# Kernel optimization log

Hardware: AMD Instinct MI355X
Metric: run time of the kernel (lower is better)

## Reference

```python
import jax, jax.numpy as jnp
import numpy as np


def group_norm(x, g, b, groups, eps=1e-5):
    # x: (B, C, H, W), PyTorch GroupNorm semantics
    B, C, H, W = x.shape
    xr = x.reshape(B, groups, -1)
    m = xr.mean(-1, keepdims=True)
    v = xr.var(-1, keepdims=True)
    xn = ((xr - m) * jax.lax.rsqrt(v + eps)).reshape(B, C, H, W)
    return xn * g[:, None, None] + b[:, None, None]


def mamba(xs, in_w, conv_w, conv_b, xproj_w, dt_w, dt_b, A_log, D, out_w):
    # Standard Mamba block: in_proj -> causal depthwise conv -> SiLU ->
    # x_proj -> softplus(dt_proj) -> selective scan -> gate -> out_proj.
    Bsz, L, d = xs.shape
    di = in_w.shape[0] // 2
    r = dt_w.shape[1]
    n = A_log.shape[1]
    K = conv_w.shape[1]
    xz = xs @ in_w.T                           # (B, L, 2*di)
    xpart, z = xz[..., :di], xz[..., di:]
    xp = jnp.pad(xpart, ((0, 0), (K - 1, 0), (0, 0)))  # causal pad
    xc = conv_b + sum(xp[:, k:k + L, :] * conv_w[:, k] for k in range(K))
    xc = jax.nn.silu(xc)
    proj = xc @ xproj_w.T                      # (B, L, r + 2n)
    dt = proj[..., :r]
    Bm = proj[..., r:r + n]
    Cm = proj[..., r + n:]
    delta = jax.nn.softplus(dt @ dt_w.T + dt_b)   # (B, L, di)
    A = -jnp.exp(A_log)                            # (di, n)
    dA = jnp.exp(jnp.einsum('bld,dn->bldn', delta, A))
    dBu = jnp.einsum('bld,bln,bld->bldn', delta, Bm, xc)

    def step(h, inp):
        dA_t, dBu_t, C_t = inp
        h = dA_t * h + dBu_t                  # (B, di, n)
        return h, jnp.einsum('bdn,bn->bd', h, C_t)

    h0 = jnp.zeros((Bsz, di, n), xs.dtype)
    _, ys = jax.lax.scan(step, h0, (jnp.moveaxis(dA, 1, 0), jnp.moveaxis(dBu, 1, 0), jnp.moveaxis(Cm, 1, 0)))
    y = jnp.moveaxis(ys, 0, 1) + D * xc
    y = y * jax.nn.silu(z)
    return y @ out_w.T


def setup_inputs() -> dict:
    def nrm(i, shape, s=0.05):
        return jax.random.normal(jax.random.fold_in(jax.random.key(0), i), shape, dtype=jnp.float32) * s

    f32 = jnp.float32
    C = 128
    di, r, n = 256, 8, 16          # spa mamba: d_model=128, expand=2
    di2, r2 = 64, 2                # spe mamba: d_model=32
    A1 = jnp.log(jnp.broadcast_to(jnp.arange(1, n + 1, dtype=f32), (di, n)))
    A2 = jnp.log(jnp.broadcast_to(jnp.arange(1, n + 1, dtype=f32), (di2, n)))
    return {
        'x': nrm(0, (2, C, 64, 64), 1.0),
        'pe_w': nrm(1, (C, C)), 'pe_b': jnp.zeros((C,), f32),
        'pe_gn_g': jnp.ones((C,), f32), 'pe_gn_b': jnp.zeros((C,), f32),
        'spa_in_w': nrm(2, (2 * di, C)),
        'spa_conv_w': nrm(3, (di, 4)), 'spa_conv_b': jnp.zeros((di,), f32),
        'spa_xproj_w': nrm(4, (r + 2 * n, di)),
        'spa_dt_w': nrm(5, (di, r)), 'spa_dt_b': jnp.full((di,), -2.0, f32),
        'spa_Alog': A1, 'spa_D': jnp.ones((di,), f32),
        'spa_out_w': nrm(6, (C, di)),
        'spa_gn_g': jnp.ones((C,), f32), 'spa_gn_b': jnp.zeros((C,), f32),
        'spe_in_w': nrm(7, (2 * di2, 32)),
        'spe_conv_w': nrm(8, (di2, 4)), 'spe_conv_b': jnp.zeros((di2,), f32),
        'spe_xproj_w': nrm(9, (r2 + 2 * n, di2)),
        'spe_dt_w': nrm(10, (di2, r2)), 'spe_dt_b': jnp.full((di2,), -2.0, f32),
        'spe_Alog': A2, 'spe_D': jnp.ones((di2,), f32),
        'spe_out_w': nrm(11, (32, di2)),
        'spe_gn_g': jnp.ones((C,), f32), 'spe_gn_b': jnp.zeros((C,), f32),
        'fuse_w': jnp.full((2,), 0.5, f32),
        'cls_w': nrm(12, (10, C)), 'cls_b': jnp.zeros((10,), f32),
        'ref_dw_w': nrm(13, (C, 1, 3, 3)),
        'ref_gn_g': jnp.ones((C,), f32), 'ref_gn_b': jnp.zeros((C,), f32),
        'ref_pw_w': nrm(14, (1, C)), 'ref_pw_b': jnp.zeros((1,), f32),
        'alpha': jnp.asarray(1e-4, f32),
    }


def reference(x, pe_w, pe_b, pe_gn_g, pe_gn_b, spa_in_w, spa_conv_w, spa_conv_b, spa_xproj_w, spa_dt_w, spa_dt_b, spa_Alog, spa_D, spa_out_w, spa_gn_g, spa_gn_b, spe_in_w, spe_conv_w, spe_conv_b, spe_xproj_w, spe_dt_w, spe_dt_b, spe_Alog, spe_D, spe_out_w, spe_gn_g, spe_gn_b, fuse_w, cls_w, cls_b, ref_dw_w, ref_gn_g, ref_gn_b, ref_pw_w, ref_pw_b, alpha):
    B, _, H, W = x.shape
    # patch embedding: 1x1 conv + GroupNorm + SiLU
    h1 = jnp.einsum('bchw,oc->bohw', x, pe_w) + pe_b[:, None, None]
    h1 = jax.nn.silu(group_norm(h1, pe_gn_g, pe_gn_b, 4))
    # SpaMamba: scan over flattened spatial tokens (B, H*W, C)
    seq = h1.transpose(0, 2, 3, 1).reshape(B, H * W, -1)
    y = mamba(seq, spa_in_w, spa_conv_w, spa_conv_b, spa_xproj_w, spa_dt_w, spa_dt_b, spa_Alog, spa_D, spa_out_w)
    y = y.reshape(B, H, W, -1).transpose(0, 3, 1, 2)
    spa = jax.nn.silu(group_norm(y, spa_gn_g, spa_gn_b, 4)) + h1
    # SpeMamba: token_num=4, group_channel_num=32, channel_num=128 (no pad)
    seq2 = h1.transpose(0, 2, 3, 1).reshape(B * H * W, 4, 32)
    y2 = mamba(seq2, spe_in_w, spe_conv_w, spe_conv_b, spe_xproj_w, spe_dt_w, spe_dt_b, spe_Alog, spe_D, spe_out_w)
    y2 = y2.reshape(B, H, W, -1).transpose(0, 3, 1, 2)
    spe = h1 + jax.nn.silu(group_norm(y2, spe_gn_g, spe_gn_b, 4))
    # attention-weighted fusion + residual (BothMamba, use_att=True)
    wts = jax.nn.softmax(fuse_w)
    feat = spa * wts[0] + spe * wts[1] + h1
    # classifier head (1x1 conv)
    logits = jnp.einsum('bchw,oc->bohw', feat, cls_w) + cls_b[:, None, None]
    # BoundaryAwareLogitRefiner
    edge = jax.lax.conv_general_dilated(feat, ref_dw_w, (1, 1), ((1, 1), (1, 1)), feature_group_count=feat.shape[1], dimension_numbers=('NCHW', 'OIHW', 'NCHW'))
    edge = jax.nn.silu(group_norm(edge, ref_gn_g, ref_gn_b, 4))
    edge = jax.nn.sigmoid(jnp.einsum('bchw,oc->bohw', edge, ref_pw_w) + ref_pw_b[:, None, None])
    local = jax.lax.reduce_window(logits, 0.0, jax.lax.add, (1, 1, 3, 3), (1, 1, 1, 1), ((0, 0), (0, 0), (1, 1), (1, 1))) / 9.0  # count_include_pad=True
    return logits + alpha * (1.0 - edge) * (local - logits)
```

## Files before the change

### kernel.cpp

```cpp
#include <hip/hip_runtime.h>
#include <math.h>

#define DEV __device__ __forceinline__

DEV float sigm(float x){ return 1.f/(1.f+__expf(-x)); }
DEV float siluf(float x){ return x * sigm(x); }
DEV float softplusf(float x){ return x > 20.f ? x : log1pf(__expf(x)); }

static constexpr float NG = 131072.0f;

static constexpr size_t WS_H1    = 0;
static constexpr size_t WS_H1PRE = 1048576;
static constexpr size_t WS_XC    = 2097152;
static constexpr size_t WS_ZSIL  = 4194304;
static constexpr size_t WS_XZ    = 6291456;
static constexpr size_t WS_DELTA = 6291456;
static constexpr size_t WS_BM    = 8388608;
static constexpr size_t WS_CM    = 8519680;
static constexpr size_t WS_LOG   = 8650752;
static constexpr size_t WS_Y     = 10485760;
static constexpr size_t WS_P     = 12582912;
static constexpr size_t WS_Q     = 13107200;
static constexpr size_t WS_HS    = 13631488;
static constexpr size_t WS_Y2    = 14155776;
static constexpr size_t WS_FEAT  = 15204352;
static constexpr size_t WS_STATS = 16252928;
static constexpr size_t WS_PEWT  = 16253056;
static constexpr size_t WS_INWT  = WS_PEWT  + 16384;
static constexpr size_t WS_OUTWT = WS_INWT  + 65536;
static constexpr size_t WS_XPWT  = WS_OUTWT + 32768;

__global__ void __launch_bounds__(256)
k_red(const float* __restrict__ part, float* __restrict__ outS, int half){
  __shared__ float red[4];
  int b = blockIdx.x >> 3, j = blockIdx.x & 7;
  float s = 0.f;
  for (int i = b*half + threadIdx.x; i < (b+1)*half; i += 256)
    s += part[(size_t)i*8 + j];
  s += __shfl_xor(s,1); s += __shfl_xor(s,2); s += __shfl_xor(s,4);
  s += __shfl_xor(s,8); s += __shfl_xor(s,16); s += __shfl_xor(s,32);
  if ((threadIdx.x & 63) == 0) red[threadIdx.x>>6] = s;
  __syncthreads();
  if (threadIdx.x == 0) outS[b*8+j] = red[0]+red[1]+red[2]+red[3];
}

__global__ void __launch_bounds__(256)
k_transpose(const float* __restrict__ pe_w, const float* __restrict__ in_w,
            const float* __restrict__ out_w, const float* __restrict__ xp_w,
            float* __restrict__ peT, float* __restrict__ inT,
            float* __restrict__ outT, float* __restrict__ xpT){
  int i0 = blockIdx.x*256 + threadIdx.x;
  int nt = gridDim.x*256;
  for (int k = i0; k < 128*128; k += nt){ int r = k >> 7, c = k & 127; peT[c*128 + r] = pe_w[k]; }
  for (int k = i0; k < 512*128; k += nt){ int r = k >> 7, c = k & 127; inT[c*512 + r] = in_w[k]; }
  for (int k = i0; k < 128*256; k += nt){ int r = k >> 8, c = k & 255; outT[c*128 + r] = out_w[k]; }
  for (int k = i0; k < 40*256;  k += nt){ int r = k >> 8, c = k & 255; xpT[c*40 + r] = xp_w[k]; }
}

__global__ void __launch_bounds__(256)
k_pe(const float* __restrict__ x, const float* __restrict__ peT,
     const float* __restrict__ pe_b, float* __restrict__ h1pre,
     float* __restrict__ part){
  __shared__ float xs[128][33];
  __shared__ float red1[4][64], red2[4][64];
  int tid = threadIdx.x;
  int m0 = blockIdx.x * 32;
  int b = m0 >> 12, pl = m0 & 4095;
  for (int i = tid; i < 32*128; i += 256){
    int t = i >> 7, c = i & 127;
    xs[c][t] = x[(size_t)(b*128 + c)*4096 + pl + t];
  }
  __syncthreads();
  int o = tid & 127, half = tid >> 7;
  float acc[16];
  #pragma unroll
  for (int t = 0; t < 16; t++) acc[t] = 0.f;
  for (int c = 0; c < 128; c++){
    float wv = peT[c*128 + o];
    const float* xr = &xs[c][half*16];
    #pragma unroll
    for (int t = 0; t < 16; t++) acc[t] += wv * xr[t];
  }
  float bo = pe_b[o];
  float s1 = 0.f, s2 = 0.f;
  for (int t = 0; t < 16; t++){
    float vv = acc[t] + bo;
    s1 += vv; s2 += vv*vv;
    h1pre[(size_t)(m0 + half*16 + t)*128 + o] = vv;
  }
  int g = o >> 5, idx = (o & 31) | (half << 5);
  red1[g][idx] = s1; red2[g][idx] = s2;
  __syncthreads();
  int rg = tid >> 6, ridx = tid & 63;
  for (int s = 32; s >= 1; s >>= 1){
    if (ridx < s){ red1[rg][ridx] += red1[rg][ridx+s]; red2[rg][ridx] += red2[rg][ridx+s]; }
    __syncthreads();
  }
  if (ridx == 0){
    part[(size_t)blockIdx.x*8 + rg*2+0] = red1[rg][0];
    part[(size_t)blockIdx.x*8 + rg*2+1] = red2[rg][0];
  }
}

__global__ void __launch_bounds__(256)
k_gnsilu(const float* __restrict__ pre, const float* __restrict__ stats,
         const float* __restrict__ gw, const float* __restrict__ gb,
         float* __restrict__ outb){
  int idx = blockIdx.x*256 + threadIdx.x;
  int c = idx & 127; int pix = idx >> 7; int b = pix >> 12; int g = c >> 5;
  float s1 = stats[(b*4+g)*2], s2 = stats[(b*4+g)*2+1];
  float m = s1 * (1.f/NG);
  float v = s2 * (1.f/NG) - m*m;
  float xn = (pre[idx] - m) * rsqrtf(v + 1e-5f);
  float val = xn * gw[c] + gb[c];
  outb[idx] = siluf(val);
}

__global__ void __launch_bounds__(256)
k_xz(const float* __restrict__ h1, const float* __restrict__ inT,
     float* __restrict__ xz){
  __shared__ float xs[128][33];
  int tid = threadIdx.x;
  int m0 = blockIdx.x * 32;
  for (int i = tid; i < 32*128; i += 256){
    int t = i >> 7, c = i & 127;
    xs[c][t] = h1[(size_t)(m0 + t)*128 + c];
  }
  __syncthreads();
  float acc0[32], acc1[32];
  #pragma unroll
  for (int t = 0; t < 32; t++){ acc0[t]=0.f; acc1[t]=0.f; }
  int o = tid;
  for (int c = 0; c < 128; c++){
    float w0 = inT[c*512 + o];
    float w1 = inT[c*512 + o + 256];
    #pragma unroll
    for (int t = 0; t < 32; t++){
      float a = xs[c][t];
      acc0[t] += w0*a; acc1[t] += w1*a;
    }
  }
  for (int t = 0; t < 32; t++){
    xz[(size_t)(m0+t)*512 + o]       = acc0[t];
    xz[(size_t)(m0+t)*512 + o + 256] = acc1[t];
  }
}

__global__ void __launch_bounds__(256)
k_conv(const float* __restrict__ xz, const float* __restrict__ cw,
       const float* __restrict__ cb, float* __restrict__ xc,
       float* __restrict__ zsil){
  int idx = blockIdx.x*256 + threadIdx.x;
  int d = idx & 255;
  int l = (idx >> 8) & 4095;
  int b = idx >> 20;
  float v = cb[d];
  #pragma unroll
  for (int k = 0; k < 4; k++){
    int ls = l - 3 + k;
    if (ls >= 0) v += xz[(size_t)(b*4096 + ls)*512 + d] * cw[d*4 + k];
  }
  xc[idx] = siluf(v);
  float z = xz[(size_t)(b*4096 + l)*512 + 256 + d];
  zsil[idx] = siluf(z);
}

__global__ void __launch_bounds__(256)
k_proj(const float* __restrict__ xc, const float* __restrict__ xpT,
       const float* __restrict__ dtw, const float* __restrict__ dtb,
       float* __restrict__ delta, float* __restrict__ Bm, float* __restrict__ Cm){
  __shared__ float xt[32][260];
  __shared__ float pr[32][40];
  int tid = threadIdx.x;
  int m0 = blockIdx.x * 32;
  for (int i = tid; i < 32*256; i += 256){
    int t = i >> 8, d = i & 255;
    xt[t][d] = xc[(size_t)(m0+t)*256 + d];
  }
  __syncthreads();
  {
    int t = tid >> 3, j0 = tid & 7;
    float a0=0.f,a1=0.f,a2=0.f,a3=0.f,a4=0.f;
    for (int d = 0; d < 256; d++){
      float xv = xt[t][d];
      const float* wp = &xpT[d*40 + j0];
      a0 += xv*wp[0]; a1 += xv*wp[8]; a2 += xv*wp[16]; a3 += xv*wp[24]; a4 += xv*wp[32];
    }
    pr[t][j0] = a0; pr[t][j0+8] = a1; pr[t][j0+16] = a2; pr[t][j0+24] = a3; pr[t][j0+32] = a4;
  }
  __syncthreads();
  {
    int d = tid;
    float w[8];
    #pragma unroll
    for (int r = 0; r < 8; r++) w[r] = dtw[d*8+r];
    float bd = dtb[d];
    for (int t = 0; t < 32; t++){
      float val = bd;
      #pragma unroll
      for (int r = 0; r < 8; r++) val += pr[t][r]*w[r];
      delta[(size_t)(m0+t)*256 + d] = softplusf(val);
    }
  }
  for (int i = tid; i < 512; i += 256){
    int t = i >> 4, n = i & 15;
    Bm[(size_t)(m0+t)*16 + n] = pr[t][8+n];
    Cm[(size_t)(m0+t)*16 + n] = pr[t][24+n];
  }
}

__global__ void __launch_bounds__(256)
k_scan1(const float* __restrict__ delta, const float* __restrict__ xc,
        const float* __restrict__ Bm, const float* __restrict__ Alog,
        float* __restrict__ P, float* __restrict__ Q){
  __shared__ float sd[64][16], sx[64][16], sb[64][16];
  int blk = blockIdx.x;
  int b = blk >> 10;
  int chunk = (blk >> 4) & 63;
  int dblk = blk & 15;
  int tid = threadIdx.x;
  size_t rowbase = (size_t)(b*4096 + chunk*64);
  for (int i = tid; i < 64*16; i += 256){
    int ii = i >> 4, dd = i & 15;
    sd[ii][dd] = delta[(rowbase + ii)*256 + dblk*16 + dd];
    sx[ii][dd] = xc  [(rowbase + ii)*256 + dblk*16 + dd];
    sb[ii][dd] = Bm  [(rowbase + ii)*16 + dd];
  }
  int dl = tid >> 4, n = tid & 15;
  int d = dblk*16 + dl;
  float An = -__expf(Alog[d*16 + n]);
  __syncthreads();
  float Pv = 1.f, Qv = 0.f;
  for (int i = 0; i < 64; i++){
    float dv = sd[i][dl];
    float a = __expf(dv * An);
    Qv = a*Qv + dv * sb[i][n] * sx[i][dl];
    Pv *= a;
  }
  size_t o = (size_t)(b*64+chunk)*4096 + dblk*256 + tid;
  P[o] = Pv; Q[o] = Qv;
}

__global__ void __launch_bounds__(256)
k_scan2(const float* __restrict__ P, const float* __restrict__ Q,
        float* __restrict__ hs){
  int gid = blockIdx.x*256 + threadIdx.x;
  int b = gid >> 12, dn = gid & 4095;
  float h = 0.f;
  for (int ch = 0; ch < 64; ch++){
    size_t idx = (size_t)(b*64 + ch)*4096 + dn;
    hs[idx] = h;
    h = P[idx]*h + Q[idx];
  }
}

__global__ void __launch_bounds__(256)
k_scan3(const float* __restrict__ delta, const float* __restrict__ xc,
        const float* __restrict__ Bm, const float* __restrict__ Cm,
        const float* __restrict__ zsil, const float* __restrict__ Alog,
        const float* __restrict__ Dv, const float* __restrict__ hs,
        float* __restrict__ y){
  __shared__ float sd[64][16], sx[64][16], sb[64][16], sc[64][16], sz[64][16], yt[64][16];
  int blk = blockIdx.x;
  int b = blk >> 10;
  int chunk = (blk >> 4) & 63;
  int dblk = blk & 15;
  int tid = threadIdx.x;
  size_t rowbase = (size_t)(b*4096 + chunk*64);
  for (int i = tid; i < 64*16; i += 256){
    int ii = i >> 4, dd = i & 15;
    sd[ii][dd] = delta[(rowbase + ii)*256 + dblk*16 + dd];
    sx[ii][dd] = xc  [(rowbase + ii)*256 + dblk*16 + dd];
    sz[ii][dd] = zsil[(rowbase + ii)*256 + dblk*16 + dd];
    sb[ii][dd] = Bm  [(rowbase + ii)*16 + dd];
    sc[ii][dd] = Cm  [(rowbase + ii)*16 + dd];
  }
  int dl = tid >> 4, n = tid & 15;
  int d = dblk*16 + dl;
  float An = -__expf(Alog[d*16 + n]);
  float h = hs[(size_t)(b*64+chunk)*4096 + dblk*256 + tid];
  float Dd = Dv[d];
  __syncthreads();
  for (int i = 0; i < 64; i++){
    float dv = sd[i][dl], xv = sx[i][dl];
    float a = __expf(dv * An);
    h = a*h + dv * sb[i][n] * xv;
    float ctr = h * sc[i][n];
    ctr += __shfl_xor(ctr, 1);
    ctr += __shfl_xor(ctr, 2);
    ctr += __shfl_xor(ctr, 4);
    ctr += __shfl_xor(ctr, 8);
    if (n == 0) yt[i][dl] = (ctr + Dd*xv) * sz[i][dl];
  }
  __syncthreads();
  for (int i = tid; i < 1024; i += 256){
    int ii = i >> 4, dd = i & 15;
    y[(rowbase + ii)*256 + dblk*16 + dd] = yt[ii][dd];
  }
}

__global__ void __launch_bounds__(256)
k_outproj(const float* __restrict__ y, const float* __restrict__ outT,
          float* __restrict__ yproj, float* __restrict__ part){
  __shared__ float ytile[256][33];
  __shared__ float red1[4][64], red2[4][64];
  int tid = threadIdx.x;
  int m0 = blockIdx.x * 32;
  for (int i = tid; i < 32*256; i += 256){
    int t = i >> 8, d = i & 255;
    ytile[d][t] = y[(size_t)(m0+t)*256 + d];
  }
  __syncthreads();
  int o = tid & 127, half = tid >> 7;
  float acc[16];
  #pragma unroll
  for (int t = 0; t < 16; t++) acc[t] = 0.f;
  for (int d = 0; d < 256; d++){
    float wv = outT[d*128 + o];
    const float* yr = &ytile[d][half*16];
    #pragma unroll
    for (int t = 0; t < 16; t++) acc[t] += wv * yr[t];
  }
  float s1 = 0.f, s2 = 0.f;
  for (int t = 0; t < 16; t++){
    float vv = acc[t];
    s1 += vv; s2 += vv*vv;
    yproj[(size_t)(m0 + half*16 + t)*128 + o] = vv;
  }
  int g = o >> 5, idx = (o & 31) | (half << 5);
  red1[g][idx] = s1; red2[g][idx] = s2;
  __syncthreads();
  int rg = tid >> 6, ridx = tid & 63;
  for (int s = 32; s >= 1; s >>= 1){
    if (ridx < s){ red1[rg][ridx] += red1[rg][ridx+s]; red2[rg][ridx] += red2[rg][ridx+s]; }
    __syncthreads();
  }
  if (ridx == 0){
    part[(size_t)blockIdx.x*8 + rg*2+0] = red1[rg][0];
    part[(size_t)blockIdx.x*8 + rg*2+1] = red2[rg][0];
  }
}

__global__ void __launch_bounds__(256)
k_spe_a(const float* __restrict__ h1, const float* __restrict__ in_w,
        const float* __restrict__ conv_w, const float* __restrict__ conv_b,
        float* __restrict__ xc2, float* __restrict__ xc2T,
        float* __restrict__ zsil2){
  __shared__ float s_in[4][128];
  int tid = threadIdx.x;
  int w = tid >> 6, lane = tid & 63;
  float wx[32], wz[32];
  {
    const float4* rx = (const float4*)(in_w + (size_t)lane*32);
    const float4* rz = (const float4*)(in_w + (size_t)(64+lane)*32);
    #pragma unroll
    for (int k = 0; k < 8; k++){
      float4 a = rx[k]; wx[k*4]=a.x; wx[k*4+1]=a.y; wx[k*4+2]=a.z; wx[k*4+3]=a.w;
      float4 b = rz[k]; wz[k*4]=b.x; wz[k*4+1]=b.y; wz[k*4+2]=b.z; wz[k*4+3]=b.w;
    }
  }
  float4 cwv = ((const float4*)conv_w)[lane];
  float cbv = conv_b[lane];
  for (int i = 0; i < 4; i++){
    int pix = blockIdx.x*16 + w*4 + i;
    float2 hv = ((const float2*)(h1 + (size_t)pix*128))[lane];
    s_in[w][2*lane] = hv.x; s_in[w][2*lane+1] = hv.y;
    float xpr[4], zs[4];
    #pragma unroll
    for (int l = 0; l < 4; l++){
      const float4* sv = (const float4*)&s_in[w][l*32];
      float ax = 0.f, az = 0.f;
      #pragma unroll
      for (int c4 = 0; c4 < 8; c4++){
        float4 v = sv[c4];
        ax += v.x*wx[c4*4] + v.y*wx[c4*4+1] + v.z*wx[c4*4+2] + v.w*wx[c4*4+3];
        az += v.x*wz[c4*4] + v.y*wz[c4*4+1] + v.z*wz[c4*4+2] + v.w*wz[c4*4+3];
      }
      xpr[l] = ax; zs[l] = siluf(az);
    }
    #pragma unroll
    for (int l = 0; l < 4; l++){
      float v = cbv;
      if (l >= 3) v += xpr[l-3]*cwv.x;
      if (l >= 2) v += xpr[l-2]*cwv.y;
      if (l >= 1) v += xpr[l-1]*cwv.z;
      v += xpr[l]*cwv.w;
      float sx = siluf(v);
      int tok = pix*4 + l;
      xc2 [(size_t)tok*64 + lane] = sx;
      xc2T[(size_t)lane*32768 + tok] = sx;
      zsil2[(size_t)tok*64 + lane] = zs[l];
    }
  }
}

__global__ void __launch_bounds__(256)
k_spe_b(const float* __restrict__ xc2T, const float* __restrict__ xpw,
        float* __restrict__ proj){
  int tok = blockIdx.x*256 + threadIdx.x;
  float xcv[64];
  #pragma unroll 64
  for (int dd = 0; dd < 64; dd++) xcv[dd] = xc2T[(size_t)dd*32768 + tok];
  float* pr = proj + (size_t)tok*36;
  #pragma unroll 2
  for (int j = 0; j < 34; j++){
    const float4* wr = (const float4*)(xpw + j*64);
    float a = 0.f;
    #pragma unroll
    for (int k = 0; k < 16; k++){
      float4 wv = wr[k];
      a += xcv[k*4]*wv.x + xcv[k*4+1]*wv.y + xcv[k*4+2]*wv.z + xcv[k*4+3]*wv.w;
    }
    pr[j] = a;
  }
}

__global__ void __launch_bounds__(256)
k_spe_c(const float* __restrict__ xc2, const float* __restrict__ zsil2,
        const float* __restrict__ proj, const float* __restrict__ dt_w,
        const float* __restrict__ dt_b, const float* __restrict__ Alog,
        const float* __restrict__ Dvec, float* __restrict__ yg){
  int tid = threadIdx.x;
  int w = tid >> 6, lane = tid & 63;
  float2 dtwv = ((const float2*)dt_w)[lane];
  float dbv = dt_b[lane], Dd = Dvec[lane];
  float An[16];
  {
    const float4* ar = (const float4*)(Alog + (size_t)lane*16);
    #pragma unroll
    for (int k = 0; k < 4; k++){
      float4 a = ar[k];
      An[k*4]   = -__expf(a.x); An[k*4+1] = -__expf(a.y);
      An[k*4+2] = -__expf(a.z); An[k*4+3] = -__expf(a.w);
    }
  }
  for (int i = 0; i < 4; i++){
    int pix = blockIdx.x*16 + w*4 + i;
    float h[16];
    #pragma unroll
    for (int n = 0; n < 16; n++) h[n] = 0.f;
    #pragma unroll
    for (int l = 0; l < 4; l++){
      int tok = pix*4 + l;
      float pj[36];
      {
        const float4* pr = (const float4*)(proj + (size_t)tok*36);
        #pragma unroll
        for (int k = 0; k < 9; k++){
          float4 v = pr[k];
          pj[k*4]=v.x; pj[k*4+1]=v.y; pj[k*4+2]=v.z; pj[k*4+3]=v.w;
        }
      }
      float xv = xc2[(size_t)tok*64 + lane];
      float zv = zsil2[(size_t)tok*64 + lane];
      float dt = softplusf(dbv + pj[0]*dtwv.x + pj[1]*dtwv.y);
      float ys = 0.f;
      #pragma unroll
      for (int n = 0; n < 16; n++){
        float a = __expf(dt * An[n]);
        h[n] = a*h[n] + dt * pj[2+n] * xv;
        ys += h[n] * pj[18+n];
      }
      yg[(size_t)tok*64 + lane] = (ys + Dd*xv) * zv;
    }
  }
}

__global__ void __launch_bounds__(256)
k_spe_d(const float* __restrict__ yg, const float* __restrict__ out_w,
        float* __restrict__ y2, float* __restrict__ part){
  __shared__ float ldsWT[64*32];
  __shared__ float bst[8];
  int tid = threadIdx.x;
  for (int i = tid; i < 2048; i += 256){
    int c2 = i >> 6, dd = i & 63;
    ldsWT[dd*32 + c2] = out_w[i];
  }
  if (tid < 8) bst[tid] = 0.f;
  __syncthreads();
  int w = tid >> 6, lane = tid & 63;
  int c2 = lane & 31, slot = lane >> 5;
  int tokbase = blockIdx.x*64 + w*16 + slot;
  float acc[8];
  #pragma unroll
  for (int i = 0; i < 8; i++) acc[i] = 0.f;
  for (int dd4 = 0; dd4 < 16; dd4++){
    float w0 = ldsWT[(dd4*4+0)*32 + c2];
    float w1 = ldsWT[(dd4*4+1)*32 + c2];
    float w2 = ldsWT[(dd4*4+2)*32 + c2];
    float w3 = ldsWT[(dd4*4+3)*32 + c2];
    #pragma unroll
    for (int i = 0; i < 8; i++){
      int tok = tokbase + 2*i;
      float4 yv = ((const float4*)(yg + (size_t)tok*64))[dd4];
      acc[i] += yv.x*w0 + yv.y*w1 + yv.z*w2 + yv.w*w3;
    }
  }
  #pragma unroll
  for (int i = 0; i < 8; i++){
    int tok = tokbase + 2*i;
    int pix = tok >> 2, l = tok & 3;
    y2[(size_t)pix*128 + l*32 + c2] = acc[i];
    float s1 = acc[i], s2 = acc[i]*acc[i];
    s1 += __shfl_xor(s1,1);  s2 += __shfl_xor(s2,1);
    s1 += __shfl_xor(s1,2);  s2 += __shfl_xor(s2,2);
    s1 += __shfl_xor(s1,4);  s2 += __shfl_xor(s2,4);
    s1 += __shfl_xor(s1,8);  s2 += __shfl_xor(s2,8);
    s1 += __shfl_xor(s1,16); s2 += __shfl_xor(s2,16);
    if (c2 == 0){
      atomicAdd(&bst[l*2+0], s1);
      atomicAdd(&bst[l*2+1], s2);
    }
  }
  __syncthreads();
  if (tid < 8) part[(size_t)blockIdx.x*8 + tid] = bst[tid];
}

__global__ void __launch_bounds__(256)
k_fuse(const float* __restrict__ h1, const float* __restrict__ yproj,
       const float* __restrict__ y2, const float* __restrict__ stats,
       const float* __restrict__ spa_g, const float* __restrict__ spa_b,
       const float* __restrict__ spe_g, const float* __restrict__ spe_b,
       const float* __restrict__ fuse_w, const float* __restrict__ cls_w,
       const float* __restrict__ cls_b, float* __restrict__ feat,
       float* __restrict__ logits){
  __shared__ float ft[2][128];
  int tid = threadIdx.x;
  int pixl = tid >> 7, c = tid & 127;
  int pix = blockIdx.x*2 + pixl;
  int b = pix >> 12, g = c >> 5;
  float m1 = stats[16 + (b*4+g)*2]   * (1.f/NG);
  float v1 = stats[16 + (b*4+g)*2+1] * (1.f/NG) - m1*m1;
  float m2 = stats[32 + (b*4+g)*2]   * (1.f/NG);
  float v2 = stats[32 + (b*4+g)*2+1] * (1.f/NG) - m2*m2;
  float h = h1[(size_t)pix*128 + c];
  float sa = siluf((yproj[(size_t)pix*128+c] - m1)*rsqrtf(v1+1e-5f)*spa_g[c] + spa_b[c]) + h;
  float sp = h + siluf((y2[(size_t)pix*128+c] - m2)*rsqrtf(v2+1e-5f)*spe_g[c] + spe_b[c]);
  float e0 = __expf(fuse_w[0]), e1 = __expf(fuse_w[1]);
  float w0 = e0/(e0+e1), w1 = e1/(e0+e1);
  float f = sa*w0 + sp*w1 + h;
  feat[(size_t)pix*128+c] = f;
  ft[pixl][c] = f;
  __syncthreads();
  if (tid < 20){
    int pl = (tid >= 10) ? 1 : 0;
    int o = tid - pl*10;
    float acc = cls_b[o];
    for (int cc = 0; cc < 128; cc++) acc += ft[pl][cc]*cls_w[o*128+cc];
    logits[(size_t)(blockIdx.x*2 + pl)*16 + o] = acc;
  }
}

__global__ void __launch_bounds__(256)
k_dw(const float* __restrict__ feat, const float* __restrict__ dww,
     float* __restrict__ epre, float* __restrict__ part){
  __shared__ float red1[4][64], red2[4][64];
  int tid = threadIdx.x;
  int pixl = tid >> 7, c = tid & 127;
  int pix = blockIdx.x*2 + pixl;
  int b = pix >> 12, p = pix & 4095, yy = p >> 6, xx = p & 63;
  float acc = 0.f;
  for (int dy = -1; dy <= 1; dy++){
    int ny = yy + dy; if (ny < 0 || ny > 63) continue;
    for (int dx = -1; dx <= 1; dx++){
      int nx = xx + dx; if (nx < 0 || nx > 63) continue;
      acc += feat[(size_t)((b<<12)|(ny<<6)|nx)*128 + c] * dww[c*9 + (dy+1)*3 + (dx+1)];
    }
  }
  epre[(size_t)pix*128 + c] = acc;
  int g = c >> 5;
  int idx = (c & 31) | (pixl << 5);
  red1[g][idx] = acc; red2[g][idx] = acc*acc;
  __syncthreads();
  int rg = tid >> 6, ridx = tid & 63;
  for (int s = 32; s >= 1; s >>= 1){
    if (ridx < s){ red1[rg][ridx] += red1[rg][ridx+s]; red2[rg][ridx] += red2[rg][ridx+s]; }
    __syncthreads();
  }
  if (ridx == 0){
    part[(size_t)blockIdx.x*8 + rg*2+0] = red1[rg][0];
    part[(size_t)blockIdx.x*8 + rg*2+1] = red2[rg][0];
  }
}

__global__ void __launch_bounds__(256)
k_final(const float* __restrict__ epre, const float* __restrict__ logits,
        const float* __restrict__ stats, const float* __restrict__ rg_g,
        const float* __restrict__ rg_b, const float* __restrict__ pw_w,
        const float* __restrict__ pw_b, const float* __restrict__ alpha,
        float* __restrict__ outp){
  __shared__ float part[4];
  __shared__ float edge_s[2];
  int tid = threadIdx.x;
  int pixl = tid >> 7, c = tid & 127;
  int pix = blockIdx.x*2 + pixl;
  int b = pix >> 12, p = pix & 4095, yy = p >> 6, xx = p & 63;
  int g = c >> 5;
  float m = stats[48 + (b*4+g)*2]   * (1.f/NG);
  float v = stats[48 + (b*4+g)*2+1] * (1.f/NG) - m*m;
  float e = epre[(size_t)pix*128+c];
  float en = siluf((e-m)*rsqrtf(v+1e-5f)*rg_g[c] + rg_b[c]);
  float pv = en * pw_w[c];
  pv += __shfl_xor(pv,1);  pv += __shfl_xor(pv,2);  pv += __shfl_xor(pv,4);
  pv += __shfl_xor(pv,8);  pv += __shfl_xor(pv,16); pv += __shfl_xor(pv,32);
  if ((tid & 63) == 0) part[tid>>6] = pv;
  __syncthreads();
  if (tid < 2) edge_s[tid] = sigm(part[tid*2] + part[tid*2+1] + pw_b[0]);
  __syncthreads();
  if (c < 10){
    float ed = edge_s[pixl];
    int o = c;
    float lg = logits[(size_t)pix*16 + o];
    float loc = 0.f;
    for (int dy = -1; dy <= 1; dy++){
      int ny = yy+dy; if (ny < 0 || ny > 63) continue;
      for (int dx = -1; dx <= 1; dx++){
        int nx = xx+dx; if (nx < 0 || nx > 63) continue;
        loc += logits[(size_t)((b<<12)|(ny<<6)|nx)*16 + o];
      }
    }
    loc *= (1.f/9.f);
    outp[(size_t)((b*10+o)<<12) + p] = lg + alpha[0]*(1.f-ed)*(loc - lg);
  }
}

extern "C" void kernel_launch(void* const* d_in, const int* in_sizes, int n_in,
                              void* d_out, int out_size, void* d_ws, size_t ws_size,
                              hipStream_t stream){
  const float* x          = (const float*)d_in[0];
  const float* pe_w       = (const float*)d_in[1];
  const float* pe_b       = (const float*)d_in[2];
  const float* pe_gn_g    = (const float*)d_in[3];
  const float* pe_gn_b    = (const float*)d_in[4];
  const float* spa_in_w   = (const float*)d_in[5];
  const float* spa_conv_w = (const float*)d_in[6];
  const float* spa_conv_b = (const float*)d_in[7];
  const float* spa_xproj_w= (const float*)d_in[8];
  const float* spa_dt_w   = (const float*)d_in[9];
  const float* spa_dt_b   = (const float*)d_in[10];
  const float* spa_Alog   = (const float*)d_in[11];
  const float* spa_D      = (const float*)d_in[12];
  const float* spa_out_w  = (const float*)d_in[13];
  const float* spa_gn_g   = (const float*)d_in[14];
  const float* spa_gn_b   = (const float*)d_in[15];
  const float* spe_in_w   = (const float*)d_in[16];
  const float* spe_conv_w = (const float*)d_in[17];
  const float* spe_conv_b = (const float*)d_in[18];
  const float* spe_xproj_w= (const float*)d_in[19];
  const float* spe_dt_w   = (const float*)d_in[20];
  const float* spe_dt_b   = (const float*)d_in[21];
  const float* spe_Alog   = (const float*)d_in[22];
  const float* spe_D      = (const float*)d_in[23];
  const float* spe_out_w  = (const float*)d_in[24];
  const float* spe_gn_g   = (const float*)d_in[25];
  const float* spe_gn_b   = (const float*)d_in[26];
  const float* fuse_w     = (const float*)d_in[27];
  const float* cls_w      = (const float*)d_in[28];
  const float* cls_b      = (const float*)d_in[29];
  const float* ref_dw_w   = (const float*)d_in[30];
  const float* ref_gn_g   = (const float*)d_in[31];
  const float* ref_gn_b   = (const float*)d_in[32];
  const float* ref_pw_w   = (const float*)d_in[33];
  const float* ref_pw_b   = (const float*)d_in[34];
  const float* alpha      = (const float*)d_in[35];
  float* ws  = (float*)d_ws;
  float* out = (float*)d_out;

  float* partPE  = ws + WS_Y;
  float* partSPA = ws + WS_HS;
  float* partSPE = ws + WS_Q;
  float* partDW  = ws + WS_P;
  float* xc2   = ws + WS_XC;
  float* xc2T  = ws + WS_ZSIL;
  float* zsil2 = ws + WS_DELTA;
  float* proj  = ws + WS_BM;
  float* yg    = ws + WS_Y;

  k_transpose<<<64,256,0,stream>>>(pe_w, spa_in_w, spa_out_w, spa_xproj_w,
      ws+WS_PEWT, ws+WS_INWT, ws+WS_OUTWT, ws+WS_XPWT);
  k_pe<<<256,256,0,stream>>>(x, ws+WS_PEWT, pe_b, ws+WS_H1PRE, partPE);
  k_red<<<16,256,0,stream>>>(partPE, ws+WS_STATS+0, 128);
  k_gnsilu<<<4096,256,0,stream>>>(ws+WS_H1PRE, ws+WS_STATS, pe_gn_g, pe_gn_b, ws+WS_H1);
  k_xz<<<256,256,0,stream>>>(ws+WS_H1, ws+WS_INWT, ws+WS_XZ);
  k_conv<<<8192,256,0,stream>>>(ws+WS_XZ, spa_conv_w, spa_conv_b, ws+WS_XC, ws+WS_ZSIL);
  k_proj<<<256,256,0,stream>>>(ws+WS_XC, ws+WS_XPWT, spa_dt_w, spa_dt_b,
      ws+WS_DELTA, ws+WS_BM, ws+WS_CM);
  k_scan1<<<2048,256,0,stream>>>(ws+WS_DELTA, ws+WS_XC, ws+WS_BM, spa_Alog, ws+WS_P, ws+WS_Q);
  k_scan2<<<32,256,0,stream>>>(ws+WS_P, ws+WS_Q, ws+WS_HS);
  k_scan3<<<2048,256,0,stream>>>(ws+WS_DELTA, ws+WS_XC, ws+WS_BM, ws+WS_CM,
      ws+WS_ZSIL, spa_Alog, spa_D, ws+WS_HS, ws+WS_Y);
  k_outproj<<<256,256,0,stream>>>(ws+WS_Y, ws+WS_OUTWT, ws+WS_H1PRE, partSPA);
  k_red<<<16,256,0,stream>>>(partSPA, ws+WS_STATS+16, 128);
  k_spe_a<<<512,256,0,stream>>>(ws+WS_H1, spe_in_w, spe_conv_w, spe_conv_b,
      xc2, xc2T, zsil2);
  k_spe_b<<<128,256,0,stream>>>(xc2T, spe_xproj_w, proj);
  k_spe_c<<<512,256,0,stream>>>(xc2, zsil2, proj, spe_dt_w, spe_dt_b,
      spe_Alog, spe_D, yg);
  k_spe_d<<<512,256,0,stream>>>(yg, spe_out_w, ws+WS_Y2, partSPE);
  k_red<<<16,256,0,stream>>>(partSPE, ws+WS_STATS+32, 256);
  k_fuse<<<4096,256,0,stream>>>(ws+WS_H1, ws+WS_H1PRE, ws+WS_Y2, ws+WS_STATS,
      spa_gn_g, spa_gn_b, spe_gn_g, spe_gn_b, fuse_w, cls_w, cls_b,
      ws+WS_FEAT, ws+WS_LOG);
  k_dw<<<4096,256,0,stream>>>(ws+WS_FEAT, ref_dw_w, ws+WS_Y, partDW);
  k_red<<<16,256,0,stream>>>(partDW, ws+WS_STATS+48, 2048);
  k_final<<<4096,256,0,stream>>>(ws+WS_Y, ws+WS_LOG, ws+WS_STATS,
      ref_gn_g, ref_gn_b, ref_pw_w, ref_pw_b, alpha, out);
  (void)in_sizes; (void)n_in; (void)out_size; (void)ws_size;
}
```

Baseline: 461.4 us.

## Retile pointwise GEMMs into 2D register-blocked tiles with vectorized loads

```diff
diff --git a/kernel.cpp b/kernel.cpp
--- a/kernel.cpp
+++ b/kernel.cpp
@@ -61,44 +61,71 @@
 k_pe(const float* __restrict__ x, const float* __restrict__ peT,
      const float* __restrict__ pe_b, float* __restrict__ h1pre,
      float* __restrict__ part){
-  __shared__ float xs[128][33];
-  __shared__ float red1[4][64], red2[4][64];
-  int tid = threadIdx.x;
-  int m0 = blockIdx.x * 32;
-  int b = m0 >> 12, pl = m0 & 4095;
-  for (int i = tid; i < 32*128; i += 256){
-    int t = i >> 7, c = i & 127;
-    xs[c][t] = x[(size_t)(b*128 + c)*4096 + pl + t];
-  }
-  __syncthreads();
-  int o = tid & 127, half = tid >> 7;
-  float acc[16];
-  #pragma unroll
-  for (int t = 0; t < 16; t++) acc[t] = 0.f;
-  for (int c = 0; c < 128; c++){
-    float wv = peT[c*128 + o];
-    const float* xr = &xs[c][half*16];
-    #pragma unroll
-    for (int t = 0; t < 16; t++) acc[t] += wv * xr[t];
-  }
-  float bo = pe_b[o];
+  __shared__ float As[16][36];
+  __shared__ float Bs[16][64];
+  __shared__ float red1[2][4], red2[2][4];
+  int tid = threadIdx.x;
+  int bx = blockIdx.x, by = blockIdx.y;
+  int m0 = bx*32, n0 = by*64;
+  int b = m0 >> 12, pl0 = m0 & 4095;
+  int tx = tid & 15, ty = tid >> 4;
+  float acc[2][4];
+  #pragma unroll
+  for (int i = 0; i < 2; i++)
+    #pragma unroll
+    for (int j = 0; j < 4; j++) acc[i][j] = 0.f;
+  for (int k0 = 0; k0 < 128; k0 += 16){
+    if (tid < 128){
+      int k = tid >> 3, mm = (tid & 7)*4;
+      float4 a = *(const float4*)(x + ((size_t)b*128 + k0+k)*4096 + pl0 + mm);
+      *(float4*)&As[k][mm] = a;
+    }
+    {
+      int k = tid >> 4, n = (tid & 15)*4;
+      *(float4*)&Bs[k][n] = *(const float4*)(peT + (size_t)(k0+k)*128 + n0+n);
+    }
+    __syncthreads();
+    #pragma unroll
+    for (int k = 0; k < 16; k++){
+      float2 av = *(const float2*)&As[k][ty*2];
+      float4 bv = *(const float4*)&Bs[k][tx*4];
+      acc[0][0] += av.x*bv.x; acc[0][1] += av.x*bv.y; acc[0][2] += av.x*bv.z; acc[0][3] += av.x*bv.w;
+      acc[1][0] += av.y*bv.x; acc[1][1] += av.y*bv.y; acc[1][2] += av.y*bv.z; acc[1][3] += av.y*bv.w;
+    }
+    __syncthreads();
+  }
+  float4 bias = *(const float4*)(pe_b + n0 + tx*4);
   float s1 = 0.f, s2 = 0.f;
-  for (int t = 0; t < 16; t++){
-    float vv = acc[t] + bo;
-    s1 += vv; s2 += vv*vv;
-    h1pre[(size_t)(m0 + half*16 + t)*128 + o] = vv;
-  }
-  int g = o >> 5, idx = (o & 31) | (half << 5);
-  red1[g][idx] = s1; red2[g][idx] = s2;
-  __syncthreads();
-  int rg = tid >> 6, ridx = tid & 63;
-  for (int s = 32; s >= 1; s >>= 1){
-    if (ridx < s){ red1[rg][ridx] += red1[rg][ridx+s]; red2[rg][ridx] += red2[rg][ridx+s]; }
-    __syncthreads();
-  }
-  if (ridx == 0){
-    part[(size_t)blockIdx.x*8 + rg*2+0] = red1[rg][0];
-    part[(size_t)blockIdx.x*8 + rg*2+1] = red2[rg][0];
+  #pragma unroll
+  for (int i = 0; i < 2; i++){
+    float4 st;
+    st.x = acc[i][0]+bias.x; st.y = acc[i][1]+bias.y;
+    st.z = acc[i][2]+bias.z; st.w = acc[i][3]+bias.w;
+    s1 += st.x+st.y+st.z+st.w;
+    s2 += st.x*st.x + st.y*st.y + st.z*st.z + st.w*st.w;
+    *(float4*)(h1pre + (size_t)(m0 + ty*2 + i)*128 + n0 + tx*4) = st;
+  }
+  s1 += __shfl_xor(s1,1);  s2 += __shfl_xor(s2,1);
+  s1 += __shfl_xor(s1,2);  s2 += __shfl_xor(s2,2);
+  s1 += __shfl_xor(s1,4);  s2 += __shfl_xor(s2,4);
+  s1 += __shfl_xor(s1,16); s2 += __shfl_xor(s2,16);
+  s1 += __shfl_xor(s1,32); s2 += __shfl_xor(s2,32);
+  int lane = tid & 63, w = tid >> 6;
+  if ((lane & 55) == 0){
+    int gl = (lane >> 3) & 1;
+    red1[gl][w] = s1; red2[gl][w] = s2;
+  }
+  __syncthreads();
+  if (tid < 8){
+    int gg = tid >> 1, which = tid & 1;
+    int gl = gg - by*2;
+    float v = 0.f;
+    if (gl == 0 || gl == 1){
+      v = which ? (red2[gl][0]+red2[gl][1]+red2[gl][2]+red2[gl][3])
+                : (red1[gl][0]+red1[gl][1]+red1[gl][2]+red1[gl][3]);
+    }
+    int pblk = b*256 + (bx & 127) + by*128;
+    part[(size_t)pblk*8 + tid] = v;
   }
 }
 
@@ -119,30 +146,42 @@
 __global__ void __launch_bounds__(256)
 k_xz(const float* __restrict__ h1, const float* __restrict__ inT,
      float* __restrict__ xz){
-  __shared__ float xs[128][33];
-  int tid = threadIdx.x;
-  int m0 = blockIdx.x * 32;
-  for (int i = tid; i < 32*128; i += 256){
-    int t = i >> 7, c = i & 127;
-    xs[c][t] = h1[(size_t)(m0 + t)*128 + c];
-  }
-  __syncthreads();
-  float acc0[32], acc1[32];
-  #pragma unroll
-  for (int t = 0; t < 32; t++){ acc0[t]=0.f; acc1[t]=0.f; }
-  int o = tid;
-  for (int c = 0; c < 128; c++){
-    float w0 = inT[c*512 + o];
-    float w1 = inT[c*512 + o + 256];
-    #pragma unroll
-    for (int t = 0; t < 32; t++){
-      float a = xs[c][t];
-      acc0[t] += w0*a; acc1[t] += w1*a;
-    }
-  }
-  for (int t = 0; t < 32; t++){
-    xz[(size_t)(m0+t)*512 + o]       = acc0[t];
-    xz[(size_t)(m0+t)*512 + o + 256] = acc1[t];
+  __shared__ float As[16][68];
+  __shared__ float Bs[16][64];
+  int tid = threadIdx.x;
+  int m0 = blockIdx.x*64, n0 = blockIdx.y*64;
+  int tx = tid & 15, ty = tid >> 4;
+  float acc[4][4];
+  #pragma unroll
+  for (int i = 0; i < 4; i++)
+    #pragma unroll
+    for (int j = 0; j < 4; j++) acc[i][j] = 0.f;
+  for (int k0 = 0; k0 < 128; k0 += 16){
+    {
+      int m = tid >> 2, kk = (tid & 3)*4;
+      float4 a = *(const float4*)(h1 + (size_t)(m0+m)*128 + k0+kk);
+      As[kk+0][m] = a.x; As[kk+1][m] = a.y; As[kk+2][m] = a.z; As[kk+3][m] = a.w;
+    }
+    {
+      int k = tid >> 4, n = (tid & 15)*4;
+      *(float4*)&Bs[k][n] = *(const float4*)(inT + (size_t)(k0+k)*512 + n0+n);
+    }
+    __syncthreads();
+    #pragma unroll
+    for (int k = 0; k < 16; k++){
+      float4 av = *(const float4*)&As[k][ty*4];
+      float4 bv = *(const float4*)&Bs[k][tx*4];
+      acc[0][0] += av.x*bv.x; acc[0][1] += av.x*bv.y; acc[0][2] += av.x*bv.z; acc[0][3] += av.x*bv.w;
+      acc[1][0] += av.y*bv.x; acc[1][1] += av.y*bv.y; acc[1][2] += av.y*bv.z; acc[1][3] += av.y*bv.w;
+      acc[2][0] += av.z*bv.x; acc[2][1] += av.z*bv.y; acc[2][2] += av.z*bv.z; acc[2][3] += av.z*bv.w;
+      acc[3][0] += av.w*bv.x; acc[3][1] += av.w*bv.y; acc[3][2] += av.w*bv.z; acc[3][3] += av.w*bv.w;
+    }
+    __syncthreads();
+  }
+  #pragma unroll
+  for (int i = 0; i < 4; i++){
+    float4 st; st.x = acc[i][0]; st.y = acc[i][1]; st.z = acc[i][2]; st.w = acc[i][3];
+    *(float4*)(xz + (size_t)(m0 + ty*4 + i)*512 + n0 + tx*4) = st;
   }
 }
 
@@ -302,42 +341,68 @@
 __global__ void __launch_bounds__(256)
 k_outproj(const float* __restrict__ y, const float* __restrict__ outT,
           float* __restrict__ yproj, float* __restrict__ part){
-  __shared__ float ytile[256][33];
-  __shared__ float red1[4][64], red2[4][64];
-  int tid = threadIdx.x;
-  int m0 = blockIdx.x * 32;
-  for (int i = tid; i < 32*256; i += 256){
-    int t = i >> 8, d = i & 255;
-    ytile[d][t] = y[(size_t)(m0+t)*256 + d];
-  }
-  __syncthreads();
-  int o = tid & 127, half = tid >> 7;
-  float acc[16];
-  #pragma unroll
-  for (int t = 0; t < 16; t++) acc[t] = 0.f;
-  for (int d = 0; d < 256; d++){
-    float wv = outT[d*128 + o];
-    const float* yr = &ytile[d][half*16];
-    #pragma unroll
-    for (int t = 0; t < 16; t++) acc[t] += wv * yr[t];
+  __shared__ float As[16][36];
+  __shared__ float Bs[16][64];
+  __shared__ float red1[2][4], red2[2][4];
+  int tid = threadIdx.x;
+  int bx = blockIdx.x, by = blockIdx.y;
+  int m0 = bx*32, n0 = by*64;
+  int b = m0 >> 12;
+  int tx = tid & 15, ty = tid >> 4;
+  float acc[2][4];
+  #pragma unroll
+  for (int i = 0; i < 2; i++)
+    #pragma unroll
+    for (int j = 0; j < 4; j++) acc[i][j] = 0.f;
+  for (int k0 = 0; k0 < 256; k0 += 16){
+    if (tid < 128){
+      int m = tid >> 2, kk = (tid & 3)*4;
+      float4 a = *(const float4*)(y + (size_t)(m0+m)*256 + k0+kk);
+      As[kk+0][m] = a.x; As[kk+1][m] = a.y; As[kk+2][m] = a.z; As[kk+3][m] = a.w;
+    }
+    {
+      int k = tid >> 4, n = (tid & 15)*4;
+      *(float4*)&Bs[k][n] = *(const float4*)(outT + (size_t)(k0+k)*128 + n0+n);
+    }
+    __syncthreads();
+    #pragma unroll
+    for (int k = 0; k < 16; k++){
+      float2 av = *(const float2*)&As[k][ty*2];
+      float4 bv = *(const float4*)&Bs[k][tx*4];
+      acc[0][0] += av.x*bv.x; acc[0][1] += av.x*bv.y; acc[0][2] += av.x*bv.z; acc[0][3] += av.x*bv.w;
+      acc[1][0] += av.y*bv.x; acc[1][1] += av.y*bv.y; acc[1][2] += av.y*bv.z; acc[1][3] += av.y*bv.w;
+    }
+    __syncthreads();
   }
   float s1 = 0.f, s2 = 0.f;
-  for (int t = 0; t < 16; t++){
-    float vv = acc[t];
-    s1 += vv; s2 += vv*vv;
-    yproj[(size_t)(m0 + half*16 + t)*128 + o] = vv;
-  }
-  int g = o >> 5, idx = (o & 31) | (half << 5);
-  red1[g][idx] = s1; red2[g][idx] = s2;
-  __syncthreads();
-  int rg = tid >> 6, ridx = tid & 63;
-  for (int s = 32; s >= 1; s >>= 1){
-    if (ridx < s){ red1[rg][ridx] += red1[rg][ridx+s]; red2[rg][ridx] += red2[rg][ridx+s]; }
-    __syncthreads();
-  }
-  if (ridx == 0){
-    part[(size_t)blockIdx.x*8 + rg*2+0] = red1[rg][0];
-    part[(size_t)blockIdx.x*8 + rg*2+1] = red2[rg][0];
+  #pragma unroll
+  for (int i = 0; i < 2; i++){
+    float4 st; st.x = acc[i][0]; st.y = acc[i][1]; st.z = acc[i][2]; st.w = acc[i][3];
+    s1 += st.x+st.y+st.z+st.w;
+    s2 += st.x*st.x + st.y*st.y + st.z*st.z + st.w*st.w;
+    *(float4*)(yproj + (size_t)(m0 + ty*2 + i)*128 + n0 + tx*4) = st;
+  }
+  s1 += __shfl_xor(s1,1);  s2 += __shfl_xor(s2,1);
+  s1 += __shfl_xor(s1,2);  s2 += __shfl_xor(s2,2);
+  s1 += __shfl_xor(s1,4);  s2 += __shfl_xor(s2,4);
+  s1 += __shfl_xor(s1,16); s2 += __shfl_xor(s2,16);
+  s1 += __shfl_xor(s1,32); s2 += __shfl_xor(s2,32);
+  int lane = tid & 63, w = tid >> 6;
+  if ((lane & 55) == 0){
+    int gl = (lane >> 3) & 1;
+    red1[gl][w] = s1; red2[gl][w] = s2;
+  }
+  __syncthreads();
+  if (tid < 8){
+    int gg = tid >> 1, which = tid & 1;
+    int gl = gg - by*2;
+    float v = 0.f;
+    if (gl == 0 || gl == 1){
+      v = which ? (red2[gl][0]+red2[gl][1]+red2[gl][2]+red2[gl][3])
+                : (red1[gl][0]+red1[gl][1]+red1[gl][2]+red1[gl][3]);
+    }
+    int pblk = b*256 + (bx & 127) + by*128;
+    part[(size_t)pblk*8 + tid] = v;
   }
 }
 
@@ -678,10 +743,10 @@
 
   k_transpose<<<64,256,0,stream>>>(pe_w, spa_in_w, spa_out_w, spa_xproj_w,
       ws+WS_PEWT, ws+WS_INWT, ws+WS_OUTWT, ws+WS_XPWT);
-  k_pe<<<256,256,0,stream>>>(x, ws+WS_PEWT, pe_b, ws+WS_H1PRE, partPE);
-  k_red<<<16,256,0,stream>>>(partPE, ws+WS_STATS+0, 128);
+  k_pe<<<dim3(256,2),256,0,stream>>>(x, ws+WS_PEWT, pe_b, ws+WS_H1PRE, partPE);
+  k_red<<<16,256,0,stream>>>(partPE, ws+WS_STATS+0, 256);
   k_gnsilu<<<4096,256,0,stream>>>(ws+WS_H1PRE, ws+WS_STATS, pe_gn_g, pe_gn_b, ws+WS_H1);
-  k_xz<<<256,256,0,stream>>>(ws+WS_H1, ws+WS_INWT, ws+WS_XZ);
+  k_xz<<<dim3(128,8),256,0,stream>>>(ws+WS_H1, ws+WS_INWT, ws+WS_XZ);
   k_conv<<<8192,256,0,stream>>>(ws+WS_XZ, spa_conv_w, spa_conv_b, ws+WS_XC, ws+WS_ZSIL);
   k_proj<<<256,256,0,stream>>>(ws+WS_XC, ws+WS_XPWT, spa_dt_w, spa_dt_b,
       ws+WS_DELTA, ws+WS_BM, ws+WS_CM);
@@ -689,8 +754,8 @@
   k_scan2<<<32,256,0,stream>>>(ws+WS_P, ws+WS_Q, ws+WS_HS);
   k_scan3<<<2048,256,0,stream>>>(ws+WS_DELTA, ws+WS_XC, ws+WS_BM, ws+WS_CM,
       ws+WS_ZSIL, spa_Alog, spa_D, ws+WS_HS, ws+WS_Y);
-  k_outproj<<<256,256,0,stream>>>(ws+WS_Y, ws+WS_OUTWT, ws+WS_H1PRE, partSPA);
-  k_red<<<16,256,0,stream>>>(partSPA, ws+WS_STATS+16, 128);
+  k_outproj<<<dim3(256,2),256,0,stream>>>(ws+WS_Y, ws+WS_OUTWT, ws+WS_H1PRE, partSPA);
+  k_red<<<16,256,0,stream>>>(partSPA, ws+WS_STATS+16, 256);
   k_spe_a<<<512,256,0,stream>>>(ws+WS_H1, spe_in_w, spe_conv_w, spe_conv_b,
       xc2, xc2T, zsil2);
   k_spe_b<<<128,256,0,stream>>>(xc2T, spe_xproj_w, proj);
```

Result: faster. 407.9 us (-11.6%).
